# Kernel tuning notes

Measured on AMD Instinct MI355X. Metric: run time of the kernel, lower is better.

The kernel has to match this reference:

```python
import jax, jax.numpy as jnp
import numpy as np

B, T, I, H, V = 32, 64, 512, 512, 32000


def setup_inputs() -> dict:
    key = jax.random.key(0)
    ks = jax.random.split(key, 8)
    s_in = 1.0 / np.sqrt(H)  # torch LSTMCell/Linear uniform init scale
    return {
        "isequence": jax.random.normal(ks[0], (B, T, I), dtype=jnp.float32),
        "hidden_t": jax.random.normal(ks[1], (B, H), dtype=jnp.float32),
        "W_ih": jax.random.uniform(ks[2], (4 * H, I), jnp.float32, -s_in, s_in),
        "W_hh": jax.random.uniform(ks[3], (4 * H, H), jnp.float32, -s_in, s_in),
        "b_ih": jax.random.uniform(ks[4], (4 * H,), jnp.float32, -s_in, s_in),
        "b_hh": jax.random.uniform(ks[5], (4 * H,), jnp.float32, -s_in, s_in),
        "W_out": jax.random.uniform(ks[6], (V, H), jnp.float32, -s_in, s_in),
        "b_out": jax.random.uniform(ks[7], (V,), jnp.float32, -s_in, s_in),
    }


def reference(isequence, hidden_t, W_ih, W_hh, b_ih, b_hh, W_out, b_out):
    # isequence: [B, T, I] -> time-major [T, B, I] (matches permute(1,0,2))
    xs = jnp.transpose(isequence, (1, 0, 2))
    # Precompute input-to-gate projections for all timesteps: [T, B, 4H]
    x_gates = jnp.einsum("tbi,gi->tbg", xs, W_ih) + b_ih + b_hh
    c0 = jnp.zeros_like(hidden_t)  # init_hidden zeros cell state

    def step(carry, xg):
        h, c = carry
        gates = xg + h @ W_hh.T  # [B, 4H], torch gate order: i, f, g, o
        i_g, f_g, g_g, o_g = jnp.split(gates, 4, axis=-1)
        i_g = jax.nn.sigmoid(i_g)
        f_g = jax.nn.sigmoid(f_g)
        g_g = jnp.tanh(g_g)
        o_g = jax.nn.sigmoid(o_g)
        c_new = f_g * c + i_g * g_g
        h_new = o_g * jnp.tanh(c_new)
        logits = h_new @ W_out.T + b_out  # [B, V]
        return (h_new, c_new), logits

    _, osequence = jax.lax.scan(step, (hidden_t, c0), x_gates)  # [T, B, V]
    return jnp.transpose(osequence, (1, 0, 2))  # [B, T, V]
```

## Files before the change

kernel.cpp:

```cpp
#include <hip/hip_runtime.h>
#include <hip/hip_bf16.h>

typedef unsigned short u16;
typedef unsigned int u32;
typedef __attribute__((ext_vector_type(4))) float f32x4;
typedef __attribute__((ext_vector_type(8))) short short8;
typedef __attribute__((ext_vector_type(4))) unsigned short u16x4;
typedef __attribute__((ext_vector_type(2))) unsigned int u32x2;
typedef __attribute__((ext_vector_type(4))) unsigned int u32x4;

#define LSTM_NBLK 16

static __device__ __forceinline__ u16 f2bf(float f) {
  union { float f; unsigned u; } v; v.f = f;
  unsigned r = v.u + 0x7FFFu + ((v.u >> 16) & 1u);
  return (u16)(r >> 16);
}

static __device__ __forceinline__ void gload_lds16(const void* g, void* l) {
  __builtin_amdgcn_global_load_lds(
      (const __attribute__((address_space(1))) unsigned int*)g,
      (__attribute__((address_space(3))) unsigned int*)l, 16, 0, 0);
}

static __device__ __forceinline__ u32x4 ld_b128u_sc(const u32* p) {
  u32x4 r;
  asm volatile("global_load_dwordx4 %0, %1, off sc0 sc1"
               : "=v"(r) : "v"(p) : "memory");
  return r;
}
static __device__ __forceinline__ void st_u64_sc(void* p, u32 lo, u32 hi) {
  u32x2 v; v[0] = lo; v[1] = hi;
  asm volatile("global_store_dwordx2 %0, %1, off sc0 sc1"
               :: "v"(p), "v"(v) : "memory");
}
static __device__ __forceinline__ void waitcnt0() {
  asm volatile("s_waitcnt vmcnt(0)" ::: "memory");
  __builtin_amdgcn_sched_barrier(0);
}

__global__ void prep_kernel(const float* __restrict__ iseq, const float* __restrict__ h0,
                            const float* __restrict__ wih, const float* __restrict__ whh,
                            const float* __restrict__ wout,
                            u16* __restrict__ wout_bf, u16* __restrict__ wih_bf,
                            u16* __restrict__ whh_bf, u16* __restrict__ ax,
                            u32* __restrict__ htag, u32* __restrict__ h2u) {
  const int S0 = 4096000;
  const int S1 = S0 + 262144;
  const int S2 = S1 + 262144;
  const int S3 = S2 + 262144;
  const int S4 = S3 + 4096;
  const int S5 = S4 + 258048;
  const int S6 = S5 + 2048;
  int u = blockIdx.x * blockDim.x + threadIdx.x;
  int stride = gridDim.x * blockDim.x;
  for (; u < S6; u += stride) {
    if (u < S0) {
      int e = u * 4; f32x4 v = *(const f32x4*)(wout + e);
      u16x4 o; o[0]=f2bf(v[0]); o[1]=f2bf(v[1]); o[2]=f2bf(v[2]); o[3]=f2bf(v[3]);
      *(u16x4*)(wout_bf + e) = o;
    } else if (u < S1) {
      int e = (u - S0) * 4; f32x4 v = *(const f32x4*)(wih + e);
      u16x4 o; o[0]=f2bf(v[0]); o[1]=f2bf(v[1]); o[2]=f2bf(v[2]); o[3]=f2bf(v[3]);
      *(u16x4*)(wih_bf + e) = o;
    } else if (u < S2) {
      int e = (u - S1) * 4; f32x4 v = *(const f32x4*)(whh + e);
      u16x4 o; o[0]=f2bf(v[0]); o[1]=f2bf(v[1]); o[2]=f2bf(v[2]); o[3]=f2bf(v[3]);
      *(u16x4*)(whh_bf + e) = o;
    } else if (u < S3) {
      int e = (u - S2) * 4; int m = e >> 9; int k = e & 511;
      int b = m & 31; int t = m >> 5;
      f32x4 v = *(const f32x4*)(iseq + ((b * 64 + t) << 9) + k);
      u16x4 o; o[0]=f2bf(v[0]); o[1]=f2bf(v[1]); o[2]=f2bf(v[2]); o[3]=f2bf(v[3]);
      *(u16x4*)(ax + e) = o;
    } else if (u < S4) {
      int e = (u - S3) * 4; f32x4 v = *(const f32x4*)(h0 + e);
      u32x4 o;
      o[0] = (1u << 16) | f2bf(v[0]); o[1] = (1u << 16) | f2bf(v[1]);
      o[2] = (1u << 16) | f2bf(v[2]); o[3] = (1u << 16) | f2bf(v[3]);
      *(u32x4*)(htag + e) = o;
    } else if (u < S5) {
      int e = (u - S4) * 4;
      u32x4 z = {0u, 0u, 0u, 0u};
      *(u32x4*)(htag + 16384 + e) = z;
    } else {
      int v = (u - S5) * 4;
      int e = v * 2;
      f32x4 x0 = *(const f32x4*)(h0 + e);
      f32x4 x1 = *(const f32x4*)(h0 + e + 4);
      u32x4 o;
      o[0] = (((u32)f2bf(x0[1])) << 16) | (u32)f2bf(x0[0]);
      o[1] = (((u32)f2bf(x0[3])) << 16) | (u32)f2bf(x0[2]);
      o[2] = (((u32)f2bf(x1[1])) << 16) | (u32)f2bf(x1[0]);
      o[3] = (((u32)f2bf(x1[3])) << 16) | (u32)f2bf(x1[2]);
      *(u32x4*)(h2u + v) = o;
    }
  }
}

__global__ __launch_bounds__(256, 2) void gemm_bt(
    const u16* __restrict__ A, const u16* __restrict__ Bw,
    float* __restrict__ C, const float* __restrict__ bias1,
    const float* __restrict__ bias2, int N, int remap) {
  __shared__ u16 As[2][8192];
  __shared__ u16 Bs[2][8192];
  const int tid = threadIdx.x;
  const int w = tid >> 6, l = tid & 63;
  const int wr = w >> 1, wc = w & 1;
  const int tm = blockIdx.y * 128, tn = blockIdx.x * 128;

  f32x4 acc[4][4];
#pragma unroll
  for (int i = 0; i < 4; ++i)
#pragma unroll
    for (int j = 0; j < 4; ++j) acc[i][j] = (f32x4){0.f, 0.f, 0.f, 0.f};

  auto stage = [&](int buf, int kt) {
#pragma unroll
    for (int i = 0; i < 4; ++i) {
      int r = (w * 4 + i) * 8 + (l >> 3);
      int c16 = (l & 7) ^ (r & 7);
      int rowm = tm + r;
      const u16* srca;
      if (remap) {
        srca = A + ((rowm & 63) + 1) * 16384 + (rowm >> 6) * 512 + kt * 64 + c16 * 8;
      } else {
        srca = A + rowm * 512 + kt * 64 + c16 * 8;
      }
      gload_lds16(srca, &As[buf][(w * 4 + i) * 512]);
      const u16* srcb = Bw + (tn + r) * 512 + kt * 64 + c16 * 8;
      gload_lds16(srcb, &Bs[buf][(w * 4 + i) * 512]);
    }
  };

  stage(0, 0);
  int buf = 0;
  for (int kt = 0; kt < 8; ++kt) {
    __syncthreads();
    if (kt < 7) stage(buf ^ 1, kt + 1);
#pragma unroll
    for (int kk = 0; kk < 2; ++kk) {
      short8 af[4], bfr[4];
#pragma unroll
      for (int mi = 0; mi < 4; ++mi) {
        int row = wr * 64 + mi * 16 + (l & 15);
        int s = (kk * 4 + (l >> 4)) ^ (row & 7);
        af[mi] = *(const short8*)&As[buf][row * 64 + s * 8];
      }
#pragma unroll
      for (int ni = 0; ni < 4; ++ni) {
        int row = wc * 64 + ni * 16 + (l & 15);
        int s = (kk * 4 + (l >> 4)) ^ (row & 7);
        bfr[ni] = *(const short8*)&Bs[buf][row * 64 + s * 8];
      }
#pragma unroll
      for (int mi = 0; mi < 4; ++mi)
#pragma unroll
        for (int ni = 0; ni < 4; ++ni)
          acc[mi][ni] = __builtin_amdgcn_mfma_f32_16x16x32_bf16(
              af[mi], bfr[ni], acc[mi][ni], 0, 0, 0);
    }
    buf ^= 1;
  }

#pragma unroll
  for (int ni = 0; ni < 4; ++ni) {
    int gcol = tn + wc * 64 + ni * 16 + (l & 15);
    float bv = 0.f;
    if (bias1) bv += bias1[gcol];
    if (bias2) bv += bias2[gcol];
#pragma unroll
    for (int mi = 0; mi < 4; ++mi) {
      int grow0 = tm + wr * 64 + mi * 16 + ((l >> 4) << 2);
      f32x4 a = acc[mi][ni];
#pragma unroll
      for (int q = 0; q < 4; ++q) {
        C[(long long)(grow0 + q) * N + gcol] = a[q] + bv;
      }
    }
  }
}

__global__ __launch_bounds__(512, 1) void lstm_persist(
    const u16* __restrict__ whh, const float* __restrict__ xg,
    u16* __restrict__ h2, u32* __restrict__ htag) {
  __shared__ u16 hbuf[2][32 * 512];
  __shared__ u16 hloc[1024];
  const int tid = threadIdx.x;
  const int w = tid >> 6, l = tid & 63;
  const int blk = blockIdx.x;
  const int j0 = (blk * 8 + w) * 4;
  const int c = l & 15;
  const int wrow = (c >> 2) * 512 + j0 + (c & 3);
  const int ko = (l >> 4) * 8;
  u32* h2u = (u32*)h2;

  short8 bfr[16];
  const u16* wp = whh + wrow * 512 + ko;
#pragma unroll
  for (int kt = 0; kt < 16; ++kt) bfr[kt] = *(const short8*)(wp + kt * 32);

  const int rq = (l >> 4) * 4;
  const int jj = l & 3;
  const int b0 = l & 15, b1 = 16 + (l & 15);
  const int s0 = b0 & 7;

  const int cb = tid & 31;
  const int ckg = tid >> 5;
  const int csw = cb & 7;

  const int pb = tid >> 4;
  const int pj = tid & 15;

  float creg[2][4];
#pragma unroll
  for (int mt = 0; mt < 2; ++mt)
#pragma unroll
    for (int q = 0; q < 4; ++q) creg[mt][q] = 0.f;

  float xcur[2][4], xnext[2][4];
#pragma unroll
  for (int mt = 0; mt < 2; ++mt)
#pragma unroll
    for (int q = 0; q < 4; ++q)
      xcur[mt][q] = xg[(mt * 16 + rq + q) * 2048 + wrow];

  for (int it = 0; it < 64; ++it) {
    u16* hb = hbuf[it & 1];
    short8 d0, d1, d2, d3;
    if (it > 0 && ckg == blk) {
      d0 = *(const short8*)&hloc[cb * 32 + 0];
      d1 = *(const short8*)&hloc[cb * 32 + 8];
      d2 = *(const short8*)&hloc[cb * 32 + 16];
      d3 = *(const short8*)&hloc[cb * 32 + 24];
    } else {
      const u32* src = htag + it * 16384 + cb * 512 + ckg * 32;
      const unsigned want = (unsigned)(it + 1);
      u32x4 a0, a1, a2, a3, a4, a5, a6, a7;
      for (;;) {
        a0 = ld_b128u_sc(src +  0); a1 = ld_b128u_sc(src +  4);
        a2 = ld_b128u_sc(src +  8); a3 = ld_b128u_sc(src + 12);
        a4 = ld_b128u_sc(src + 16); a5 = ld_b128u_sc(src + 20);
        a6 = ld_b128u_sc(src + 24); a7 = ld_b128u_sc(src + 28);
        waitcnt0();
        unsigned d = 0;
#pragma unroll
        for (int q2 = 0; q2 < 4; ++q2) {
          d |= (a0[q2] >> 16) ^ want; d |= (a1[q2] >> 16) ^ want;
          d |= (a2[q2] >> 16) ^ want; d |= (a3[q2] >> 16) ^ want;
          d |= (a4[q2] >> 16) ^ want; d |= (a5[q2] >> 16) ^ want;
          d |= (a6[q2] >> 16) ^ want; d |= (a7[q2] >> 16) ^ want;
        }
        if (d == 0) break;
      }
      d0[0]=(short)a0[0]; d0[1]=(short)a0[1]; d0[2]=(short)a0[2]; d0[3]=(short)a0[3];
      d0[4]=(short)a1[0]; d0[5]=(short)a1[1]; d0[6]=(short)a1[2]; d0[7]=(short)a1[3];
      d1[0]=(short)a2[0]; d1[1]=(short)a2[1]; d1[2]=(short)a2[2]; d1[3]=(short)a2[3];
      d1[4]=(short)a3[0]; d1[5]=(short)a3[1]; d1[6]=(short)a3[2]; d1[7]=(short)a3[3];
      d2[0]=(short)a4[0]; d2[1]=(short)a4[1]; d2[2]=(short)a4[2]; d2[3]=(short)a4[3];
      d2[4]=(short)a5[0]; d2[5]=(short)a5[1]; d2[6]=(short)a5[2]; d2[7]=(short)a5[3];
      d3[0]=(short)a6[0]; d3[1]=(short)a6[1]; d3[2]=(short)a6[2]; d3[3]=(short)a6[3];
      d3[4]=(short)a7[0]; d3[5]=(short)a7[1]; d3[6]=(short)a7[2]; d3[7]=(short)a7[3];
    }
    *(short8*)&hb[cb * 512 + (((ckg * 4 + 0) ^ csw) * 8)] = d0;
    *(short8*)&hb[cb * 512 + (((ckg * 4 + 1) ^ csw) * 8)] = d1;
    *(short8*)&hb[cb * 512 + (((ckg * 4 + 2) ^ csw) * 8)] = d2;
    *(short8*)&hb[cb * 512 + (((ckg * 4 + 3) ^ csw) * 8)] = d3;
    __syncthreads();

    f32x4 acc0 = (f32x4){0.f, 0.f, 0.f, 0.f};
    f32x4 acc1 = (f32x4){0.f, 0.f, 0.f, 0.f};
#pragma unroll
    for (int kt = 0; kt < 16; ++kt) {
      int x = ((kt * 4 + (l >> 4)) ^ s0) * 8;
      short8 a0 = *(const short8*)&hb[b0 * 512 + x];
      short8 a1 = *(const short8*)&hb[b1 * 512 + x];
      acc0 = __builtin_amdgcn_mfma_f32_16x16x32_bf16(a0, bfr[kt], acc0, 0, 0, 0);
      acc1 = __builtin_amdgcn_mfma_f32_16x16x32_bf16(a1, bfr[kt], acc1, 0, 0, 0);
    }
    if (it < 63) {
#pragma unroll
      for (int mt = 0; mt < 2; ++mt)
#pragma unroll
        for (int q = 0; q < 4; ++q)
          xnext[mt][q] = xg[((it + 1) * 32 + mt * 16 + rq + q) * 2048 + wrow];
    }

#pragma unroll
    for (int mt = 0; mt < 2; ++mt) {
#pragma unroll
      for (int q = 0; q < 4; ++q) {
        float av = (mt == 0) ? acc0[q] : acc1[q];
        float gp = av + xcur[mt][q];
        int bl = (l & 48) | jj;
        float xi = __shfl(gp, bl);
        float xf = __shfl(gp, bl | 4);
        float xgg = __shfl(gp, bl | 8);
        float xo = __shfl(gp, bl | 12);
        float is = 1.f / (1.f + __expf(-xi));
        float fs = 1.f / (1.f + __expf(-xf));
        float e2 = __expf(2.f * xgg);
        float gt = 1.f - 2.f / (e2 + 1.f);
        float os = 1.f / (1.f + __expf(-xo));
        float cn = fs * creg[mt][q] + is * gt;
        creg[mt][q] = cn;
        float e2c = __expf(2.f * cn);
        float hn = os * (1.f - 2.f / (e2c + 1.f));
        if ((l & 12) == 0) {
          int b = mt * 16 + rq + q;
          hloc[b * 32 + w * 4 + jj] = f2bf(hn);
        }
      }
    }
    __syncthreads();

    {
      u32 lo = (u32)hloc[pb * 32 + pj * 2];
      u32 hi = (u32)hloc[pb * 32 + pj * 2 + 1];
      h2u[(it + 1) * 8192 + pb * 256 + blk * 16 + pj] = (hi << 16) | lo;
      if (it < 63) {
        u32 tag = ((u32)(it + 2)) << 16;
        st_u64_sc(htag + (it + 1) * 16384 + pb * 512 + blk * 32 + pj * 2,
                  tag | lo, tag | hi);
      }
    }
    if (it < 63) {
#pragma unroll
      for (int mt = 0; mt < 2; ++mt)
#pragma unroll
        for (int q = 0; q < 4; ++q)
          xcur[mt][q] = xnext[mt][q];
    }
  }
}

extern "C" void kernel_launch(void* const* d_in, const int* in_sizes, int n_in,
                              void* d_out, int out_size, void* d_ws, size_t ws_size,
                              hipStream_t stream) {
  (void)in_sizes; (void)n_in; (void)out_size; (void)ws_size;
  const float* iseq = (const float*)d_in[0];
  const float* h0   = (const float*)d_in[1];
  const float* wih  = (const float*)d_in[2];
  const float* whh  = (const float*)d_in[3];
  const float* bih  = (const float*)d_in[4];
  const float* bhh  = (const float*)d_in[5];
  const float* wout = (const float*)d_in[6];
  const float* bout = (const float*)d_in[7];

  char* ws = (char*)d_ws;
  u16* wout_bf = (u16*)(ws + 0);
  u16* wih_bf  = (u16*)(ws + 32768000);
  u16* whh_bf  = (u16*)(ws + 34865152);
  u16* ax      = (u16*)(ws + 36962304);
  u16* h2      = (u16*)(ws + 39059456);
  u32* htag    = (u32*)(ws + 41189376);
  float* xg    = (float*)(ws + 45383680);
  float* out   = (float*)d_out;

  prep_kernel<<<4096, 256, 0, stream>>>(iseq, h0, wih, whh, wout,
                                        wout_bf, wih_bf, whh_bf, ax,
                                        htag, (u32*)h2);
  gemm_bt<<<dim3(16, 16), 256, 0, stream>>>(ax, wih_bf, xg, bih, bhh, 2048, 0);
  lstm_persist<<<LSTM_NBLK, 512, 0, stream>>>(whh_bf, xg, h2, htag);
  gemm_bt<<<dim3(250, 16), 256, 0, stream>>>(h2, wout_bf, out, bout, nullptr, 32000, 1);
}
```

Before: 649.7 us.

## Halve persistent LSTM blocks to 8 with 1024 threads and block-contiguous tagged h layout

Reorganises the persistent recurrent kernel from 16 workgroups of 512 threads to 8 workgroups of 1024 threads, so each workgroup owns 64 hidden units and fewer workgroups take part in the cross-block spin-wait exchange each step. The tagged hidden-state buffer is relaid out contiguously per producer block so stores become 128-bit writes, and each thread polls 64 bytes instead of 128. Half the threads write the tagged exchange while the other half write the bf16 h output, splitting that stage's stores. Single-buffered LDS and removal of the x-gate prefetch add a per-step global load latency on the critical path and reduce the overlap between steps.

```diff
diff --git a/kernel.cpp b/kernel.cpp
--- a/kernel.cpp
+++ b/kernel.cpp
@@ -9,7 +9,7 @@
 typedef __attribute__((ext_vector_type(2))) unsigned int u32x2;
 typedef __attribute__((ext_vector_type(4))) unsigned int u32x4;
 
-#define LSTM_NBLK 16
+#define LSTM_NBLK 8
 
 static __device__ __forceinline__ u16 f2bf(float f) {
   union { float f; unsigned u; } v; v.f = f;
@@ -29,9 +29,8 @@
                : "=v"(r) : "v"(p) : "memory");
   return r;
 }
-static __device__ __forceinline__ void st_u64_sc(void* p, u32 lo, u32 hi) {
-  u32x2 v; v[0] = lo; v[1] = hi;
-  asm volatile("global_store_dwordx2 %0, %1, off sc0 sc1"
+static __device__ __forceinline__ void st_b128u_sc(void* p, u32x4 v) {
+  asm volatile("global_store_dwordx4 %0, %1, off sc0 sc1"
                :: "v"(p), "v"(v) : "memory");
 }
 static __device__ __forceinline__ void waitcnt0() {
@@ -74,7 +73,12 @@
       u16x4 o; o[0]=f2bf(v[0]); o[1]=f2bf(v[1]); o[2]=f2bf(v[2]); o[3]=f2bf(v[3]);
       *(u16x4*)(ax + e) = o;
     } else if (u < S4) {
-      int e = (u - S3) * 4; f32x4 v = *(const f32x4*)(h0 + e);
+      int e = (u - S3) * 4;
+      int blkp = e >> 11;
+      int r = e & 2047;
+      int b = r >> 6;
+      int jl = r & 63;
+      f32x4 v = *(const f32x4*)(h0 + b * 512 + blkp * 64 + jl);
       u32x4 o;
       o[0] = (1u << 16) | f2bf(v[0]); o[1] = (1u << 16) | f2bf(v[1]);
       o[2] = (1u << 16) | f2bf(v[2]); o[3] = (1u << 16) | f2bf(v[3]);
@@ -181,15 +185,15 @@
   }
 }
 
-__global__ __launch_bounds__(512, 1) void lstm_persist(
+__global__ __launch_bounds__(1024, 1) void lstm_persist(
     const u16* __restrict__ whh, const float* __restrict__ xg,
     u16* __restrict__ h2, u32* __restrict__ htag) {
-  __shared__ u16 hbuf[2][32 * 512];
-  __shared__ u16 hloc[1024];
+  __shared__ u16 hbuf[32 * 512];
+  __shared__ u16 hloc[32 * 64];
   const int tid = threadIdx.x;
   const int w = tid >> 6, l = tid & 63;
   const int blk = blockIdx.x;
-  const int j0 = (blk * 8 + w) * 4;
+  const int j0 = blk * 64 + w * 4;
   const int c = l & 15;
   const int wrow = (c >> 2) * 512 + j0 + (c & 3);
   const int ko = (l >> 4) * 8;
@@ -205,12 +209,16 @@
   const int b0 = l & 15, b1 = 16 + (l & 15);
   const int s0 = b0 & 7;
 
-  const int cb = tid & 31;
-  const int ckg = tid >> 5;
-  const int csw = cb & 7;
-
-  const int pb = tid >> 4;
-  const int pj = tid & 15;
+  const int sw_base = tid * 16;
+  const int sw_blkp = tid >> 7;
+  const int sw_b = (sw_base & 2047) >> 6;
+  const int sw_jl = sw_base & 63;
+  const int sw_x0 = (sw_blkp * 64 + sw_jl) >> 3;
+  const int sw_swz = sw_b & 7;
+  const bool own = (sw_blkp == blk);
+
+  const int pb = (tid & 511) >> 4;
+  const int pj4 = (tid & 15) * 4;
 
   float creg[2][4];
 #pragma unroll
@@ -218,54 +226,43 @@
 #pragma unroll
     for (int q = 0; q < 4; ++q) creg[mt][q] = 0.f;
 
-  float xcur[2][4], xnext[2][4];
-#pragma unroll
-  for (int mt = 0; mt < 2; ++mt)
-#pragma unroll
-    for (int q = 0; q < 4; ++q)
-      xcur[mt][q] = xg[(mt * 16 + rq + q) * 2048 + wrow];
-
   for (int it = 0; it < 64; ++it) {
-    u16* hb = hbuf[it & 1];
-    short8 d0, d1, d2, d3;
-    if (it > 0 && ckg == blk) {
-      d0 = *(const short8*)&hloc[cb * 32 + 0];
-      d1 = *(const short8*)&hloc[cb * 32 + 8];
-      d2 = *(const short8*)&hloc[cb * 32 + 16];
-      d3 = *(const short8*)&hloc[cb * 32 + 24];
+    short8 plo, phi;
+    if (own && it > 0) {
+      plo = *(const short8*)&hloc[sw_b * 64 + sw_jl];
+      phi = *(const short8*)&hloc[sw_b * 64 + sw_jl + 8];
     } else {
-      const u32* src = htag + it * 16384 + cb * 512 + ckg * 32;
+      const u32* src = htag + it * 16384 + sw_base;
       const unsigned want = (unsigned)(it + 1);
-      u32x4 a0, a1, a2, a3, a4, a5, a6, a7;
+      u32x4 a0, a1, a2, a3;
       for (;;) {
-        a0 = ld_b128u_sc(src +  0); a1 = ld_b128u_sc(src +  4);
-        a2 = ld_b128u_sc(src +  8); a3 = ld_b128u_sc(src + 12);
-        a4 = ld_b128u_sc(src + 16); a5 = ld_b128u_sc(src + 20);
-        a6 = ld_b128u_sc(src + 24); a7 = ld_b128u_sc(src + 28);
+        a0 = ld_b128u_sc(src + 0);
+        a1 = ld_b128u_sc(src + 4);
+        a2 = ld_b128u_sc(src + 8);
+        a3 = ld_b128u_sc(src + 12);
         waitcnt0();
         unsigned d = 0;
 #pragma unroll
         for (int q2 = 0; q2 < 4; ++q2) {
           d |= (a0[q2] >> 16) ^ want; d |= (a1[q2] >> 16) ^ want;
           d |= (a2[q2] >> 16) ^ want; d |= (a3[q2] >> 16) ^ want;
-          d |= (a4[q2] >> 16) ^ want; d |= (a5[q2] >> 16) ^ want;
-          d |= (a6[q2] >> 16) ^ want; d |= (a7[q2] >> 16) ^ want;
         }
         if (d == 0) break;
       }
-      d0[0]=(short)a0[0]; d0[1]=(short)a0[1]; d0[2]=(short)a0[2]; d0[3]=(short)a0[3];
-      d0[4]=(short)a1[0]; d0[5]=(short)a1[1]; d0[6]=(short)a1[2]; d0[7]=(short)a1[3];
-      d1[0]=(short)a2[0]; d1[1]=(short)a2[1]; d1[2]=(short)a2[2]; d1[3]=(short)a2[3];
-      d1[4]=(short)a3[0]; d1[5]=(short)a3[1]; d1[6]=(short)a3[2]; d1[7]=(short)a3[3];
-      d2[0]=(short)a4[0]; d2[1]=(short)a4[1]; d2[2]=(short)a4[2]; d2[3]=(short)a4[3];
-      d2[4]=(short)a5[0]; d2[5]=(short)a5[1]; d2[6]=(short)a5[2]; d2[7]=(short)a5[3];
-      d3[0]=(short)a6[0]; d3[1]=(short)a6[1]; d3[2]=(short)a6[2]; d3[3]=(short)a6[3];
-      d3[4]=(short)a7[0]; d3[5]=(short)a7[1]; d3[6]=(short)a7[2]; d3[7]=(short)a7[3];
-    }
-    *(short8*)&hb[cb * 512 + (((ckg * 4 + 0) ^ csw) * 8)] = d0;
-    *(short8*)&hb[cb * 512 + (((ckg * 4 + 1) ^ csw) * 8)] = d1;
-    *(short8*)&hb[cb * 512 + (((ckg * 4 + 2) ^ csw) * 8)] = d2;
-    *(short8*)&hb[cb * 512 + (((ckg * 4 + 3) ^ csw) * 8)] = d3;
+      plo[0]=(short)a0[0]; plo[1]=(short)a0[1]; plo[2]=(short)a0[2]; plo[3]=(short)a0[3];
+      plo[4]=(short)a1[0]; plo[5]=(short)a1[1]; plo[6]=(short)a1[2]; plo[7]=(short)a1[3];
+      phi[0]=(short)a2[0]; phi[1]=(short)a2[1]; phi[2]=(short)a2[2]; phi[3]=(short)a2[3];
+      phi[4]=(short)a3[0]; phi[5]=(short)a3[1]; phi[6]=(short)a3[2]; phi[7]=(short)a3[3];
+    }
+    float xc[2][4];
+#pragma unroll
+    for (int mt = 0; mt < 2; ++mt)
+#pragma unroll
+      for (int q = 0; q < 4; ++q)
+        xc[mt][q] = xg[(it * 32 + mt * 16 + rq + q) * 2048 + wrow];
+
+    *(short8*)&hbuf[sw_b * 512 + ((sw_x0 ^ sw_swz) * 8)] = plo;
+    *(short8*)&hbuf[sw_b * 512 + (((sw_x0 + 1) ^ sw_swz) * 8)] = phi;
     __syncthreads();
 
     f32x4 acc0 = (f32x4){0.f, 0.f, 0.f, 0.f};
@@ -273,25 +270,18 @@
 #pragma unroll
     for (int kt = 0; kt < 16; ++kt) {
       int x = ((kt * 4 + (l >> 4)) ^ s0) * 8;
-      short8 a0 = *(const short8*)&hb[b0 * 512 + x];
-      short8 a1 = *(const short8*)&hb[b1 * 512 + x];
+      short8 a0 = *(const short8*)&hbuf[b0 * 512 + x];
+      short8 a1 = *(const short8*)&hbuf[b1 * 512 + x];
       acc0 = __builtin_amdgcn_mfma_f32_16x16x32_bf16(a0, bfr[kt], acc0, 0, 0, 0);
       acc1 = __builtin_amdgcn_mfma_f32_16x16x32_bf16(a1, bfr[kt], acc1, 0, 0, 0);
     }
-    if (it < 63) {
-#pragma unroll
-      for (int mt = 0; mt < 2; ++mt)
-#pragma unroll
-        for (int q = 0; q < 4; ++q)
-          xnext[mt][q] = xg[((it + 1) * 32 + mt * 16 + rq + q) * 2048 + wrow];
-    }
 
 #pragma unroll
     for (int mt = 0; mt < 2; ++mt) {
 #pragma unroll
       for (int q = 0; q < 4; ++q) {
         float av = (mt == 0) ? acc0[q] : acc1[q];
-        float gp = av + xcur[mt][q];
+        float gp = av + xc[mt][q];
         int bl = (l & 48) | jj;
         float xi = __shfl(gp, bl);
         float xf = __shfl(gp, bl | 4);
@@ -308,28 +298,27 @@
         float hn = os * (1.f - 2.f / (e2c + 1.f));
         if ((l & 12) == 0) {
           int b = mt * 16 + rq + q;
-          hloc[b * 32 + w * 4 + jj] = f2bf(hn);
+          hloc[b * 64 + w * 4 + jj] = f2bf(hn);
         }
       }
     }
     __syncthreads();
 
-    {
-      u32 lo = (u32)hloc[pb * 32 + pj * 2];
-      u32 hi = (u32)hloc[pb * 32 + pj * 2 + 1];
-      h2u[(it + 1) * 8192 + pb * 256 + blk * 16 + pj] = (hi << 16) | lo;
+    if (tid < 512) {
       if (it < 63) {
         u32 tag = ((u32)(it + 2)) << 16;
-        st_u64_sc(htag + (it + 1) * 16384 + pb * 512 + blk * 32 + pj * 2,
-                  tag | lo, tag | hi);
-      }
-    }
-    if (it < 63) {
-#pragma unroll
-      for (int mt = 0; mt < 2; ++mt)
-#pragma unroll
-        for (int q = 0; q < 4; ++q)
-          xcur[mt][q] = xnext[mt][q];
+        u32x4 o;
+        o[0] = tag | (u32)hloc[pb * 64 + pj4 + 0];
+        o[1] = tag | (u32)hloc[pb * 64 + pj4 + 1];
+        o[2] = tag | (u32)hloc[pb * 64 + pj4 + 2];
+        o[3] = tag | (u32)hloc[pb * 64 + pj4 + 3];
+        st_b128u_sc(htag + (it + 1) * 16384 + blk * 2048 + pb * 64 + pj4, o);
+      }
+    } else {
+      u32 lo2 = ((u32)hloc[pb * 64 + pj4 + 1] << 16) | (u32)hloc[pb * 64 + pj4 + 0];
+      u32 hi2 = ((u32)hloc[pb * 64 + pj4 + 3] << 16) | (u32)hloc[pb * 64 + pj4 + 2];
+      u32x2 v2; v2[0] = lo2; v2[1] = hi2;
+      *(u32x2*)&h2u[(it + 1) * 8192 + pb * 256 + blk * 32 + (pj4 >> 1)] = v2;
     }
   }
 }
@@ -361,6 +350,6 @@
                                         wout_bf, wih_bf, whh_bf, ax,
                                         htag, (u32*)h2);
   gemm_bt<<<dim3(16, 16), 256, 0, stream>>>(ax, wih_bf, xg, bih, bhh, 2048, 0);
-  lstm_persist<<<LSTM_NBLK, 512, 0, stream>>>(whh_bf, xg, h2, htag);
+  lstm_persist<<<LSTM_NBLK, 1024, 0, stream>>>(whh_bf, xg, h2, htag);
   gemm_bt<<<dim3(250, 16), 256, 0, stream>>>(h2, wout_bf, out, bout, nullptr, 32000, 1);
 }
```

Result: slower. 807.8 us (+24.3%).
